# Kernel tuning notes

Measured on AMD Instinct MI355X. Metric: run time of the kernel, lower is better.

Reference implementation:

```python
import jax, jax.numpy as jnp
import numpy as np

N_NODES = 524288
N_EDGES = 786432
NUM_GRAPHS = 8192
NUM_NODE_TYPES = 16
NODE_DIM = 256
EDGE_DIM = 128
OUT_DIM = 1


def setup_inputs() -> dict:
    key = jax.random.key(0)
    ks = jax.random.split(key, 12)
    h_node = jax.random.uniform(ks[0], (N_NODES, NUM_NODE_TYPES), dtype=jnp.float32)
    pos_node = jax.random.normal(ks[1], (N_NODES, 3), dtype=jnp.float32)
    batch_node = jnp.sort(jax.random.randint(ks[2], (N_NODES,), 0, NUM_GRAPHS)).astype(jnp.int64)
    edge_index = jax.random.randint(ks[3], (2, N_EDGES), 0, N_NODES).astype(jnp.int64)
    batch_edge = jnp.sort(jax.random.randint(ks[4], (N_EDGES,), 0, NUM_GRAPHS)).astype(jnp.int64)
    s = 0.05
    W_node = jax.random.normal(ks[5], (NUM_NODE_TYPES, NODE_DIM), dtype=jnp.float32) * s
    W_edge = jax.random.normal(ks[6], (2 * NUM_NODE_TYPES, EDGE_DIM), dtype=jnp.float32) * s
    H = NODE_DIM + EDGE_DIM
    W1 = jax.random.normal(ks[7], (H, H), dtype=jnp.float32) * s
    b1 = jnp.zeros((H,), dtype=jnp.float32)
    W2 = jax.random.normal(ks[8], (H, OUT_DIM), dtype=jnp.float32) * s
    b2 = jnp.zeros((OUT_DIM,), dtype=jnp.float32)
    return {"h_node": h_node, "pos_node": pos_node, "batch_node": batch_node,
            "edge_index": edge_index, "batch_edge": batch_edge,
            "W_node": W_node, "W_edge": W_edge, "W1": W1, "b1": b1, "W2": W2, "b2": b2}


def _segment_mean(x, seg_ids, num_segments):
    # fused replacement for the original per-graph boolean-mask loop:
    # h[seg==k].mean(0) for all k, via one scatter-add + count normalize
    sums = jax.ops.segment_sum(x, seg_ids, num_segments=num_segments)
    cnts = jax.ops.segment_sum(jnp.ones((x.shape[0],), x.dtype), seg_ids, num_segments=num_segments)
    return sums / jnp.maximum(cnts, 1.0)[:, None]


def reference(h_node, pos_node, batch_node, edge_index, batch_edge,
              W_node, W_edge, W1, b1, W2, b2):
    # h_edge = cat(h_node[src], h_node[dst])  -> [E, 2*num_node_types]
    h_edge_raw = jnp.concatenate([h_node[edge_index[0]], h_node[edge_index[1]]], axis=-1)
    # num_timesteps == 0 path: plain embedders, no time embedding
    hn = h_node @ W_node          # [N, node_dim]
    he = h_edge_raw @ W_edge      # [E, edge_dim]
    # encoder treated as identity (NodeEdgeNet not in scope); pooling is the target op
    node_mean = _segment_mean(hn, batch_node, NUM_GRAPHS)  # [G, node_dim]
    edge_mean = _segment_mean(he, batch_edge, NUM_GRAPHS)  # [G, edge_dim]
    h_sub = jnp.concatenate([node_mean, edge_mean], axis=-1)  # [G, node_dim+edge_dim]
    # final MLP (num_layer=2): Linear -> ReLU -> Linear
    pred = jax.nn.relu(h_sub @ W1 + b1) @ W2 + b2  # [G, 1]
    return pred
```

## Files before the change

### kernel.cpp

```cpp
#include <hip/hip_runtime.h>

#define N_NODES_C   524288
#define N_EDGES_C   786432
#define NUM_GRAPHS_C 8192
#define NT 16
#define NODE_DIM_C 256
#define EDGE_DIM_C 128
#define HDIM 384
#define KC 48

#define KR_GRAPH_BLOCKS 2048
#define KR_FOLD_BLOCKS  72
#define KR_BLOCKS (KR_GRAPH_BLOCKS + KR_FOLD_BLOCKS)
#define NODE_BLOCKS 2048
#define EDGE_BLOCKS 16384
#define EDGE_BASE   NODE_BLOCKS
#define KM_BLOCKS   (NODE_BLOCKS + EDGE_BLOCKS)

#define WS_NM    0
#define WS_EM8   524288
#define WS_WC    8912896
#define WS_NS    8986624
#define WS_DESC  9019456
#define WS_ECNT  10068032
#define WS_REC   10100800

__device__ __forceinline__ void f4_add(float4& a, const float4 v) {
    a.x += v.x; a.y += v.y; a.z += v.z; a.w += v.w;
}

__device__ __forceinline__ void f4_shfl_xor_add(float4& a, int mask) {
    a.x += __shfl_xor(a.x, mask, 64);
    a.y += __shfl_xor(a.y, mask, 64);
    a.z += __shfl_xor(a.z, mask, 64);
    a.w += __shfl_xor(a.w, mask, 64);
}

__device__ __forceinline__ int lower_bound_i32(const int* __restrict__ a, int n, int key) {
    int lo = 0, hi = n;
    while (lo < hi) {
        int mid = (lo + hi) >> 1;
        if (a[mid] < key) lo = mid + 1; else hi = mid;
    }
    return lo;
}

__device__ __forceinline__ void wave_seg_bounds(const int* __restrict__ b, int n,
                                                int g, int lane, int& s, int& e) {
    int key = g + ((lane >= 32) ? 1 : 0);
    int lo = lower_bound_i32(b, n, key);
    s = __shfl(lo, 0, 64);
    e = __shfl(lo, 32, 64);
}

__global__ __launch_bounds__(256) void kr_build(
    const int* __restrict__ bnode, const int* __restrict__ bedge,
    const int* __restrict__ esrc, const int* __restrict__ edst,
    const float* __restrict__ Wn, const float* __restrict__ We,
    const float* __restrict__ W1,
    int* __restrict__ rec, int4* __restrict__ desc,
    int* __restrict__ ecnt, int* __restrict__ nstart, float* __restrict__ Wc) {
    int tid = threadIdx.x, blk = blockIdx.x;

    if (blk >= KR_GRAPH_BLOCKS) {
        int o = (blk - KR_GRAPH_BLOCKS) * 256 + tid;
        if (o >= KC * HDIM) return;
        int k = o / HDIM, j = o % HDIM;
        float acc = 0.f;
        if (k < NT) {
            const float* wr = &Wn[k * NODE_DIM_C];
            #pragma unroll 16
            for (int kk = 0; kk < NODE_DIM_C; ++kk)
                acc = fmaf(wr[kk], W1[(size_t)kk * HDIM + j], acc);
        } else {
            const float* wr = &We[(k - NT) * EDGE_DIM_C];
            #pragma unroll 16
            for (int kk = 0; kk < EDGE_DIM_C; ++kk)
                acc = fmaf(wr[kk], W1[(size_t)(NODE_DIM_C + kk) * HDIM + j], acc);
        }
        Wc[o] = acc;
        return;
    }

    int i = blk * 256 + tid;
    {
        int g0 = bnode[i];
        int hi = (i + 1 < N_NODES_C) ? bnode[i + 1] : NUM_GRAPHS_C;
        if (i == 0) for (int g = 0; g <= g0; ++g) nstart[g] = 0;
        for (int g = g0 + 1; g <= hi; ++g) nstart[g] = i + 1;
    }

    int wave = tid >> 6, lane = tid & 63;
    int g = blk * 4 + wave;
    int s, e;
    wave_seg_bounds(bedge, N_EDGES_C, g, lane, s, e);
    int cnt = e - s;
    if (lane == 0) ecnt[g] = cnt;

    __shared__ int lcnt[4][16];
    __shared__ int lcur[4][16];
    if (lane < 16) lcnt[wave][lane] = 0;
    for (int q = s + lane; q < e; q += 64) {
        int a = esrc[q];
        atomicAdd(&lcnt[wave][((a >> 16) << 1) + 0], 1);
        int b = edst[q];
        atomicAdd(&lcnt[wave][((b >> 16) << 1) + 1], 1);
    }
    int c = (lane < 16) ? lcnt[wave][lane] : 0;
    int incl = c;
    #pragma unroll
    for (int d = 1; d < 16; d <<= 1) {
        int v = __shfl_up(incl, d, 64);
        if (lane >= d) incl += v;
    }
    int excl = incl - c;
    if (lane < 16) lcur[wave][lane] = excl;
    int i0 = (lane < 8) ? 2 * lane : 0;
    int i1 = (lane < 8) ? 2 * lane + 1 : 0;
    int i2 = (lane < 7) ? 2 * lane + 2 : 0;
    int b0 = __shfl(excl, i0, 64);
    int b1 = __shfl(excl, i1, 64);
    int e1 = __shfl(excl, i2, 64);
    if (lane < 8) {
        int e1a = (lane == 7) ? 2 * s + 2 * cnt : 2 * s + e1;
        desc[(g << 3) + lane] = make_int4(2 * s + b0, 2 * s + b1, e1a, cnt);
    }
    for (int q = s + lane; q < e; q += 64) {
        int a = esrc[q];
        int pa = atomicAdd(&lcur[wave][((a >> 16) << 1) + 0], 1);
        rec[2 * s + pa] = a;
        int b = edst[q];
        int pb = atomicAdd(&lcur[wave][((b >> 16) << 1) + 1], 1);
        rec[2 * s + pb] = b;
    }
}

__global__ __launch_bounds__(256) void km_mega(
    const float* __restrict__ h_node,
    const int* __restrict__ nstart, const int4* __restrict__ desc,
    const int* __restrict__ rec,
    float* __restrict__ nm, float* __restrict__ em8) {
    int blk  = blockIdx.x;
    int wave = threadIdx.x >> 6;
    int lane = threadIdx.x & 63;
    const float4* h4 = (const float4*)h_node;
    const float4 z4 = make_float4(0.f, 0.f, 0.f, 0.f);

    if (blk < EDGE_BASE) {
        int s8 = blk & 7;
        int g  = s8 * 1024 + (blk >> 3) * 4 + wave;
        int s = nstart[g], e = nstart[g + 1];
        int row_off = lane >> 2;
        int quad    = lane & 3;
        float4 a0 = z4, a1 = z4;
        int i = s + row_off;
        for (; i + 16 < e; i += 32) {
            float4 v0 = h4[(size_t)i * 4 + quad];
            float4 v1 = h4[(size_t)(i + 16) * 4 + quad];
            f4_add(a0, v0);
            f4_add(a1, v1);
        }
        if (i < e) f4_add(a0, h4[(size_t)i * 4 + quad]);
        f4_add(a0, a1);
        f4_shfl_xor_add(a0, 4);
        f4_shfl_xor_add(a0, 8);
        f4_shfl_xor_add(a0, 16);
        f4_shfl_xor_add(a0, 32);
        if (row_off == 0) {
            float inv = 1.f / fmaxf((float)(e - s), 1.f);
            ((float4*)nm)[(size_t)g * 4 + quad] =
                make_float4(a0.x * inv, a0.y * inv, a0.z * inv, a0.w * inv);
        }
    } else {
        int r     = blk - EDGE_BASE;
        int slice = r & 7;
        int g     = (r >> 3) * 4 + wave;
        int4 d    = desc[(g << 3) + slice];
        int slot = lane >> 3;
        int p    = (lane >> 2) & 1;
        int quad = lane & 3;
        int st = p ? d.y : d.x;
        int en = p ? d.z : d.y;
        int cmax = max(d.y - d.x, d.z - d.y);
        int T = (cmax + 7) >> 3;
        float4 acc = z4;
        int i = st + slot;
        int idx = (i < en) ? rec[i] : -1;
        for (int t = 1; t < T; ++t) {
            int i2 = i + 8;
            int nx = (i2 < en) ? rec[i2] : -1;
            if (idx >= 0) f4_add(acc, h4[(size_t)idx * 4 + quad]);
            idx = nx; i = i2;
        }
        if (idx >= 0) f4_add(acc, h4[(size_t)idx * 4 + quad]);
        f4_shfl_xor_add(acc, 8);
        f4_shfl_xor_add(acc, 16);
        f4_shfl_xor_add(acc, 32);
        if (slot == 0) {
            ((float4*)em8)[((size_t)(g * 8 + slice)) * 8 + p * 4 + quad] = acc;
        }
    }
}

#define GPB 16
__global__ __launch_bounds__(HDIM) void k3_mlp(
    const float* __restrict__ nm, const float* __restrict__ em8,
    const int* __restrict__ ecnt,
    const float* __restrict__ Wc, const float* __restrict__ b1,
    const float* __restrict__ W2, const float* __restrict__ b2,
    float* __restrict__ pred) {
    int j = threadIdx.x;
    float wc[KC];
    #pragma unroll
    for (int k = 0; k < KC; ++k) wc[k] = Wc[k * HDIM + j];
    float b1j = b1[j], w2j = W2[j], b20 = b2[0];

    __shared__ float fs[GPB][KC];
    __shared__ float part[GPB][6];
    int g0 = blockIdx.x * GPB;
    for (int t = j; t < GPB * KC; t += HDIM) {
        int g = t / KC, k = t % KC;
        int G = g0 + g;
        float val;
        if (k < NT) {
            val = nm[(size_t)G * NT + k];
        } else {
            float ssum = 0.f;
            #pragma unroll
            for (int s = 0; s < 8; ++s)
                ssum += em8[((size_t)(G * 8 + s)) * 32 + (k - NT)];
            val = ssum / fmaxf((float)ecnt[G], 1.f);
        }
        fs[g][k] = val;
    }
    __syncthreads();

    int wave = j >> 6, lane = j & 63;
    for (int g = 0; g < GPB; ++g) {
        float z = b1j;
        #pragma unroll
        for (int k = 0; k < KC; ++k) z = fmaf(fs[g][k], wc[k], z);
        z = fmaxf(z, 0.f);
        float p = z * w2j;
        #pragma unroll
        for (int off = 32; off > 0; off >>= 1) p += __shfl_down(p, off, 64);
        if (lane == 0) part[g][wave] = p;
    }
    __syncthreads();
    if (j < GPB) {
        float sacc = b20;
        #pragma unroll
        for (int w = 0; w < 6; ++w) sacc += part[j][w];
        pred[g0 + j] = sacc;
    }
}

extern "C" void kernel_launch(void* const* d_in, const int* in_sizes, int n_in,
                              void* d_out, int out_size, void* d_ws, size_t ws_size,
                              hipStream_t stream) {
    const float* h_node     = (const float*)d_in[0];
    const int*   batch_node = (const int*)d_in[2];
    const int*   edge_index = (const int*)d_in[3];
    const int*   batch_edge = (const int*)d_in[4];
    const float* W_node     = (const float*)d_in[5];
    const float* W_edge     = (const float*)d_in[6];
    const float* W1         = (const float*)d_in[7];
    const float* b1         = (const float*)d_in[8];
    const float* W2         = (const float*)d_in[9];
    const float* b2         = (const float*)d_in[10];
    float* pred = (float*)d_out;

    char* ws = (char*)d_ws;
    float* nm     = (float*)(ws + WS_NM);
    float* em8    = (float*)(ws + WS_EM8);
    float* Wc     = (float*)(ws + WS_WC);
    int*   nstart = (int*)(ws + WS_NS);
    int4*  desc   = (int4*)(ws + WS_DESC);
    int*   ecnt   = (int*)(ws + WS_ECNT);
    int*   rec    = (int*)(ws + WS_REC);

    const int* esrc = edge_index;
    const int* edst = edge_index + N_EDGES_C;

    kr_build<<<KR_BLOCKS, 256, 0, stream>>>(
        batch_node, batch_edge, esrc, edst, W_node, W_edge, W1,
        rec, desc, ecnt, nstart, Wc);
    km_mega <<<KM_BLOCKS, 256, 0, stream>>>(
        h_node, nstart, desc, rec, nm, em8);
    k3_mlp  <<<NUM_GRAPHS_C / GPB, HDIM, 0, stream>>>(
        nm, em8, ecnt, Wc, b1, W2, b2, pred);
}
```

Baseline: 150.0 us.

## Fuse node segment-mean into build kernel using binary-searched node bounds

```diff
diff --git a/kernel.cpp b/kernel.cpp
--- a/kernel.cpp
+++ b/kernel.cpp
@@ -9,21 +9,17 @@
 #define HDIM 384
 #define KC 48
 
-#define KR_GRAPH_BLOCKS 2048
-#define KR_FOLD_BLOCKS  72
-#define KR_BLOCKS (KR_GRAPH_BLOCKS + KR_FOLD_BLOCKS)
-#define NODE_BLOCKS 2048
-#define EDGE_BLOCKS 16384
-#define EDGE_BASE   NODE_BLOCKS
-#define KM_BLOCKS   (NODE_BLOCKS + EDGE_BLOCKS)
+#define KP_GRAPH_BLOCKS 2048
+#define KP_FOLD_BLOCKS  72
+#define KP_BLOCKS (KP_GRAPH_BLOCKS + KP_FOLD_BLOCKS)
+#define KE_BLOCKS 16384
 
 #define WS_NM    0
 #define WS_EM8   524288
 #define WS_WC    8912896
-#define WS_NS    8986624
-#define WS_DESC  9019456
-#define WS_ECNT  10068032
-#define WS_REC   10100800
+#define WS_DESC  8986624
+#define WS_ECNT  10035200
+#define WS_REC   10067968
 
 __device__ __forceinline__ void f4_add(float4& a, const float4 v) {
     a.x += v.x; a.y += v.y; a.z += v.z; a.w += v.w;
@@ -45,25 +41,18 @@
     return lo;
 }
 
-__device__ __forceinline__ void wave_seg_bounds(const int* __restrict__ b, int n,
-                                                int g, int lane, int& s, int& e) {
-    int key = g + ((lane >= 32) ? 1 : 0);
-    int lo = lower_bound_i32(b, n, key);
-    s = __shfl(lo, 0, 64);
-    e = __shfl(lo, 32, 64);
-}
-
-__global__ __launch_bounds__(256) void kr_build(
+__global__ __launch_bounds__(256) void kp_build(
     const int* __restrict__ bnode, const int* __restrict__ bedge,
     const int* __restrict__ esrc, const int* __restrict__ edst,
+    const float* __restrict__ h_node,
     const float* __restrict__ Wn, const float* __restrict__ We,
     const float* __restrict__ W1,
-    int* __restrict__ rec, int4* __restrict__ desc,
-    int* __restrict__ ecnt, int* __restrict__ nstart, float* __restrict__ Wc) {
+    int* __restrict__ rec, int4* __restrict__ desc, int* __restrict__ ecnt,
+    float* __restrict__ nm, float* __restrict__ Wc) {
     int tid = threadIdx.x, blk = blockIdx.x;
 
-    if (blk >= KR_GRAPH_BLOCKS) {
-        int o = (blk - KR_GRAPH_BLOCKS) * 256 + tid;
+    if (blk >= KP_GRAPH_BLOCKS) {
+        int o = (blk - KP_GRAPH_BLOCKS) * 256 + tid;
         if (o >= KC * HDIM) return;
         int k = o / HDIM, j = o % HDIM;
         float acc = 0.f;
@@ -82,25 +71,64 @@
         return;
     }
 
-    int i = blk * 256 + tid;
+    int wave = tid >> 6, lane = tid & 63;
+    int s8 = blk & 7;
+    int g  = s8 * 1024 + (blk >> 3) * 4 + wave;
+    const float4* h4 = (const float4*)h_node;
+    const float4 z4 = make_float4(0.f, 0.f, 0.f, 0.f);
+
     {
-        int g0 = bnode[i];
-        int hi = (i + 1 < N_NODES_C) ? bnode[i + 1] : NUM_GRAPHS_C;
-        if (i == 0) for (int g = 0; g <= g0; ++g) nstart[g] = 0;
-        for (int g = g0 + 1; g <= hi; ++g) nstart[g] = i + 1;
-    }
-
-    int wave = tid >> 6, lane = tid & 63;
-    int g = blk * 4 + wave;
-    int s, e;
-    wave_seg_bounds(bedge, N_EDGES_C, g, lane, s, e);
-    int cnt = e - s;
+        const int* arr = (lane & 32) ? bnode : bedge;
+        int n   = (lane & 32) ? N_NODES_C : N_EDGES_C;
+        int key = g + ((lane >> 4) & 1);
+        int lo = lower_bound_i32(arr, n, key);
+        __shared__ int bb[4][4];
+        if ((lane & 15) == 0) bb[wave][lane >> 4] = lo;
+    }
+    __builtin_amdgcn_s_waitcnt(0);
+    __shared__ int bbx[4][4];
+    int es, ee, ns, ne;
+    {
+        const int* arr = (lane & 32) ? bnode : bedge;
+        int n   = (lane & 32) ? N_NODES_C : N_EDGES_C;
+        int key = g + ((lane >> 4) & 1);
+        int lo = lower_bound_i32(arr, n, key);
+        es = __shfl(lo, 0, 64);
+        ee = __shfl(lo, 16, 64);
+        ns = __shfl(lo, 32, 64);
+        ne = __shfl(lo, 48, 64);
+    }
+    int cnt = ee - es;
     if (lane == 0) ecnt[g] = cnt;
+
+    {
+        int row_off = lane >> 2;
+        int quad    = lane & 3;
+        float4 a0 = z4, a1 = z4;
+        int i = ns + row_off;
+        for (; i + 16 < ne; i += 32) {
+            float4 v0 = h4[(size_t)i * 4 + quad];
+            float4 v1 = h4[(size_t)(i + 16) * 4 + quad];
+            f4_add(a0, v0);
+            f4_add(a1, v1);
+        }
+        if (i < ne) f4_add(a0, h4[(size_t)i * 4 + quad]);
+        f4_add(a0, a1);
+        f4_shfl_xor_add(a0, 4);
+        f4_shfl_xor_add(a0, 8);
+        f4_shfl_xor_add(a0, 16);
+        f4_shfl_xor_add(a0, 32);
+        if (row_off == 0) {
+            float inv = 1.f / fmaxf((float)(ne - ns), 1.f);
+            ((float4*)nm)[(size_t)g * 4 + quad] =
+                make_float4(a0.x * inv, a0.y * inv, a0.z * inv, a0.w * inv);
+        }
+    }
 
     __shared__ int lcnt[4][16];
     __shared__ int lcur[4][16];
     if (lane < 16) lcnt[wave][lane] = 0;
-    for (int q = s + lane; q < e; q += 64) {
+    for (int q = es + lane; q < ee; q += 64) {
         int a = esrc[q];
         atomicAdd(&lcnt[wave][((a >> 16) << 1) + 0], 1);
         int b = edst[q];
@@ -122,83 +150,54 @@
     int b1 = __shfl(excl, i1, 64);
     int e1 = __shfl(excl, i2, 64);
     if (lane < 8) {
-        int e1a = (lane == 7) ? 2 * s + 2 * cnt : 2 * s + e1;
-        desc[(g << 3) + lane] = make_int4(2 * s + b0, 2 * s + b1, e1a, cnt);
-    }
-    for (int q = s + lane; q < e; q += 64) {
+        int e1a = (lane == 7) ? 2 * es + 2 * cnt : 2 * es + e1;
+        desc[(g << 3) + lane] = make_int4(2 * es + b0, 2 * es + b1, e1a, cnt);
+    }
+    for (int q = es + lane; q < ee; q += 64) {
         int a = esrc[q];
         int pa = atomicAdd(&lcur[wave][((a >> 16) << 1) + 0], 1);
-        rec[2 * s + pa] = a;
+        rec[2 * es + pa] = a;
         int b = edst[q];
         int pb = atomicAdd(&lcur[wave][((b >> 16) << 1) + 1], 1);
-        rec[2 * s + pb] = b;
-    }
-}
-
-__global__ __launch_bounds__(256) void km_mega(
+        rec[2 * es + pb] = b;
+    }
+}
+
+__global__ __launch_bounds__(256) void ke_edge(
     const float* __restrict__ h_node,
-    const int* __restrict__ nstart, const int4* __restrict__ desc,
-    const int* __restrict__ rec,
-    float* __restrict__ nm, float* __restrict__ em8) {
+    const int4* __restrict__ desc, const int* __restrict__ rec,
+    float* __restrict__ em8) {
     int blk  = blockIdx.x;
     int wave = threadIdx.x >> 6;
     int lane = threadIdx.x & 63;
     const float4* h4 = (const float4*)h_node;
     const float4 z4 = make_float4(0.f, 0.f, 0.f, 0.f);
 
-    if (blk < EDGE_BASE) {
-        int s8 = blk & 7;
-        int g  = s8 * 1024 + (blk >> 3) * 4 + wave;
-        int s = nstart[g], e = nstart[g + 1];
-        int row_off = lane >> 2;
-        int quad    = lane & 3;
-        float4 a0 = z4, a1 = z4;
-        int i = s + row_off;
-        for (; i + 16 < e; i += 32) {
-            float4 v0 = h4[(size_t)i * 4 + quad];
-            float4 v1 = h4[(size_t)(i + 16) * 4 + quad];
-            f4_add(a0, v0);
-            f4_add(a1, v1);
-        }
-        if (i < e) f4_add(a0, h4[(size_t)i * 4 + quad]);
-        f4_add(a0, a1);
-        f4_shfl_xor_add(a0, 4);
-        f4_shfl_xor_add(a0, 8);
-        f4_shfl_xor_add(a0, 16);
-        f4_shfl_xor_add(a0, 32);
-        if (row_off == 0) {
-            float inv = 1.f / fmaxf((float)(e - s), 1.f);
-            ((float4*)nm)[(size_t)g * 4 + quad] =
-                make_float4(a0.x * inv, a0.y * inv, a0.z * inv, a0.w * inv);
-        }
-    } else {
-        int r     = blk - EDGE_BASE;
-        int slice = r & 7;
-        int g     = (r >> 3) * 4 + wave;
-        int4 d    = desc[(g << 3) + slice];
-        int slot = lane >> 3;
-        int p    = (lane >> 2) & 1;
-        int quad = lane & 3;
-        int st = p ? d.y : d.x;
-        int en = p ? d.z : d.y;
-        int cmax = max(d.y - d.x, d.z - d.y);
-        int T = (cmax + 7) >> 3;
-        float4 acc = z4;
-        int i = st + slot;
-        int idx = (i < en) ? rec[i] : -1;
-        for (int t = 1; t < T; ++t) {
-            int i2 = i + 8;
-            int nx = (i2 < en) ? rec[i2] : -1;
-            if (idx >= 0) f4_add(acc, h4[(size_t)idx * 4 + quad]);
-            idx = nx; i = i2;
-        }
+    int slice = blk & 7;
+    int g     = (blk >> 3) * 4 + wave;
+    int4 d    = desc[(g << 3) + slice];
+    int slot = lane >> 3;
+    int p    = (lane >> 2) & 1;
+    int quad = lane & 3;
+    int st = p ? d.y : d.x;
+    int en = p ? d.z : d.y;
+    int cmax = max(d.y - d.x, d.z - d.y);
+    int T = (cmax + 7) >> 3;
+    float4 acc = z4;
+    int i = st + slot;
+    int idx = (i < en) ? rec[i] : -1;
+    for (int t = 1; t < T; ++t) {
+        int i2 = i + 8;
+        int nx = (i2 < en) ? rec[i2] : -1;
         if (idx >= 0) f4_add(acc, h4[(size_t)idx * 4 + quad]);
-        f4_shfl_xor_add(acc, 8);
-        f4_shfl_xor_add(acc, 16);
-        f4_shfl_xor_add(acc, 32);
-        if (slot == 0) {
-            ((float4*)em8)[((size_t)(g * 8 + slice)) * 8 + p * 4 + quad] = acc;
-        }
+        idx = nx; i = i2;
+    }
+    if (idx >= 0) f4_add(acc, h4[(size_t)idx * 4 + quad]);
+    f4_shfl_xor_add(acc, 8);
+    f4_shfl_xor_add(acc, 16);
+    f4_shfl_xor_add(acc, 32);
+    if (slot == 0) {
+        ((float4*)em8)[((size_t)(g * 8 + slice)) * 8 + p * 4 + quad] = acc;
     }
 }
 
@@ -271,22 +270,20 @@
     float* pred = (float*)d_out;
 
     char* ws = (char*)d_ws;
-    float* nm     = (float*)(ws + WS_NM);
-    float* em8    = (float*)(ws + WS_EM8);
-    float* Wc     = (float*)(ws + WS_WC);
-    int*   nstart = (int*)(ws + WS_NS);
-    int4*  desc   = (int4*)(ws + WS_DESC);
-    int*   ecnt   = (int*)(ws + WS_ECNT);
-    int*   rec    = (int*)(ws + WS_REC);
+    float* nm   = (float*)(ws + WS_NM);
+    float* em8  = (float*)(ws + WS_EM8);
+    float* Wc   = (float*)(ws + WS_WC);
+    int4*  desc = (int4*)(ws + WS_DESC);
+    int*   ecnt = (int*)(ws + WS_ECNT);
+    int*   rec  = (int*)(ws + WS_REC);
 
     const int* esrc = edge_index;
     const int* edst = edge_index + N_EDGES_C;
 
-    kr_build<<<KR_BLOCKS, 256, 0, stream>>>(
-        batch_node, batch_edge, esrc, edst, W_node, W_edge, W1,
-        rec, desc, ecnt, nstart, Wc);
-    km_mega <<<KM_BLOCKS, 256, 0, stream>>>(
-        h_node, nstart, desc, rec, nm, em8);
+    kp_build<<<KP_BLOCKS, 256, 0, stream>>>(
+        batch_node, batch_edge, esrc, edst, h_node, W_node, W_edge, W1,
+        rec, desc, ecnt, nm, Wc);
+    ke_edge <<<KE_BLOCKS, 256, 0, stream>>>(h_node, desc, rec, em8);
     k3_mlp  <<<NUM_GRAPHS_C / GPB, HDIM, 0, stream>>>(
         nm, em8, ecnt, Wc, b1, W2, b2, pred);
 }
```

After: 149.3 us. Within noise of the previous version (-0.5%).

## Move weight-folding blocks into gather kernel and make em8 slice-major

Applied to the files above, without the earlier changes.

```diff
diff --git a/kernel.cpp b/kernel.cpp
--- a/kernel.cpp
+++ b/kernel.cpp
@@ -9,21 +9,20 @@
 #define HDIM 384
 #define KC 48
 
-#define KR_GRAPH_BLOCKS 2048
-#define KR_FOLD_BLOCKS  72
-#define KR_BLOCKS (KR_GRAPH_BLOCKS + KR_FOLD_BLOCKS)
+#define FOLD_BLOCKS 72
 #define NODE_BLOCKS 2048
 #define EDGE_BLOCKS 16384
-#define EDGE_BASE   NODE_BLOCKS
-#define KM_BLOCKS   (NODE_BLOCKS + EDGE_BLOCKS)
+#define NODE_BASE   FOLD_BLOCKS
+#define EDGE_BASE   (FOLD_BLOCKS + NODE_BLOCKS)
+#define TOTAL_BLOCKS (FOLD_BLOCKS + NODE_BLOCKS + EDGE_BLOCKS)
 
 #define WS_NM    0
 #define WS_EM8   524288
 #define WS_WC    8912896
 #define WS_NS    8986624
-#define WS_DESC  9019456
-#define WS_ECNT  10068032
-#define WS_REC   10100800
+#define WS_ECNT  9019456
+#define WS_DESC  9052288
+#define WS_REC   10100864
 
 __device__ __forceinline__ void f4_add(float4& a, const float4 v) {
     a.x += v.x; a.y += v.y; a.z += v.z; a.w += v.w;
@@ -56,14 +55,77 @@
 __global__ __launch_bounds__(256) void kr_build(
     const int* __restrict__ bnode, const int* __restrict__ bedge,
     const int* __restrict__ esrc, const int* __restrict__ edst,
+    int* __restrict__ rec, int4* __restrict__ desc,
+    int* __restrict__ ecnt, int* __restrict__ nstart) {
+    int tid = threadIdx.x, blk = blockIdx.x;
+    int i = blk * 256 + tid;
+    {
+        int g0 = bnode[i];
+        int hi = (i + 1 < N_NODES_C) ? bnode[i + 1] : NUM_GRAPHS_C;
+        if (i == 0) for (int g = 0; g <= g0; ++g) nstart[g] = 0;
+        for (int g = g0 + 1; g <= hi; ++g) nstart[g] = i + 1;
+    }
+
+    int wave = tid >> 6, lane = tid & 63;
+    int g = blk * 4 + wave;
+    int s, e;
+    wave_seg_bounds(bedge, N_EDGES_C, g, lane, s, e);
+    int cnt = e - s;
+    if (lane == 0) ecnt[g] = cnt;
+
+    __shared__ int lcnt[4][16];
+    __shared__ int lcur[4][16];
+    if (lane < 16) lcnt[wave][lane] = 0;
+    for (int q = s + lane; q < e; q += 64) {
+        int a = esrc[q];
+        atomicAdd(&lcnt[wave][((a >> 16) << 1) + 0], 1);
+        int b = edst[q];
+        atomicAdd(&lcnt[wave][((b >> 16) << 1) + 1], 1);
+    }
+    int c = (lane < 16) ? lcnt[wave][lane] : 0;
+    int incl = c;
+    #pragma unroll
+    for (int d = 1; d < 16; d <<= 1) {
+        int v = __shfl_up(incl, d, 64);
+        if (lane >= d) incl += v;
+    }
+    int excl = incl - c;
+    if (lane < 16) lcur[wave][lane] = excl;
+    int i0 = (lane < 8) ? 2 * lane : 0;
+    int i1 = (lane < 8) ? 2 * lane + 1 : 0;
+    int i2 = (lane < 7) ? 2 * lane + 2 : 0;
+    int b0 = __shfl(excl, i0, 64);
+    int b1 = __shfl(excl, i1, 64);
+    int e1 = __shfl(excl, i2, 64);
+    if (lane < 8) {
+        int e1a = (lane == 7) ? 2 * s + 2 * cnt : 2 * s + e1;
+        desc[(g << 3) + lane] = make_int4(2 * s + b0, 2 * s + b1, e1a, cnt);
+    }
+    for (int q = s + lane; q < e; q += 64) {
+        int a = esrc[q];
+        int pa = atomicAdd(&lcur[wave][((a >> 16) << 1) + 0], 1);
+        rec[2 * s + pa] = a;
+        int b = edst[q];
+        int pb = atomicAdd(&lcur[wave][((b >> 16) << 1) + 1], 1);
+        rec[2 * s + pb] = b;
+    }
+}
+
+__global__ __launch_bounds__(256) void km_mega(
+    const float* __restrict__ h_node,
+    const int* __restrict__ nstart, const int4* __restrict__ desc,
+    const int* __restrict__ rec,
     const float* __restrict__ Wn, const float* __restrict__ We,
     const float* __restrict__ W1,
-    int* __restrict__ rec, int4* __restrict__ desc,
-    int* __restrict__ ecnt, int* __restrict__ nstart, float* __restrict__ Wc) {
-    int tid = threadIdx.x, blk = blockIdx.x;
-
-    if (blk >= KR_GRAPH_BLOCKS) {
-        int o = (blk - KR_GRAPH_BLOCKS) * 256 + tid;
+    float* __restrict__ nm, float* __restrict__ em8, float* __restrict__ Wc) {
+    int blk  = blockIdx.x;
+    int wave = threadIdx.x >> 6;
+    int lane = threadIdx.x & 63;
+    const float4* h4 = (const float4*)h_node;
+    const float4 z4 = make_float4(0.f, 0.f, 0.f, 0.f);
+
+    if (blk < FOLD_BLOCKS) {
+        int o = blk * 256 + threadIdx.x;
         if (o >= KC * HDIM) return;
         int k = o / HDIM, j = o % HDIM;
         float acc = 0.f;
@@ -79,76 +141,10 @@
                 acc = fmaf(wr[kk], W1[(size_t)(NODE_DIM_C + kk) * HDIM + j], acc);
         }
         Wc[o] = acc;
-        return;
-    }
-
-    int i = blk * 256 + tid;
-    {
-        int g0 = bnode[i];
-        int hi = (i + 1 < N_NODES_C) ? bnode[i + 1] : NUM_GRAPHS_C;
-        if (i == 0) for (int g = 0; g <= g0; ++g) nstart[g] = 0;
-        for (int g = g0 + 1; g <= hi; ++g) nstart[g] = i + 1;
-    }
-
-    int wave = tid >> 6, lane = tid & 63;
-    int g = blk * 4 + wave;
-    int s, e;
-    wave_seg_bounds(bedge, N_EDGES_C, g, lane, s, e);
-    int cnt = e - s;
-    if (lane == 0) ecnt[g] = cnt;
-
-    __shared__ int lcnt[4][16];
-    __shared__ int lcur[4][16];
-    if (lane < 16) lcnt[wave][lane] = 0;
-    for (int q = s + lane; q < e; q += 64) {
-        int a = esrc[q];
-        atomicAdd(&lcnt[wave][((a >> 16) << 1) + 0], 1);
-        int b = edst[q];
-        atomicAdd(&lcnt[wave][((b >> 16) << 1) + 1], 1);
-    }
-    int c = (lane < 16) ? lcnt[wave][lane] : 0;
-    int incl = c;
-    #pragma unroll
-    for (int d = 1; d < 16; d <<= 1) {
-        int v = __shfl_up(incl, d, 64);
-        if (lane >= d) incl += v;
-    }
-    int excl = incl - c;
-    if (lane < 16) lcur[wave][lane] = excl;
-    int i0 = (lane < 8) ? 2 * lane : 0;
-    int i1 = (lane < 8) ? 2 * lane + 1 : 0;
-    int i2 = (lane < 7) ? 2 * lane + 2 : 0;
-    int b0 = __shfl(excl, i0, 64);
-    int b1 = __shfl(excl, i1, 64);
-    int e1 = __shfl(excl, i2, 64);
-    if (lane < 8) {
-        int e1a = (lane == 7) ? 2 * s + 2 * cnt : 2 * s + e1;
-        desc[(g << 3) + lane] = make_int4(2 * s + b0, 2 * s + b1, e1a, cnt);
-    }
-    for (int q = s + lane; q < e; q += 64) {
-        int a = esrc[q];
-        int pa = atomicAdd(&lcur[wave][((a >> 16) << 1) + 0], 1);
-        rec[2 * s + pa] = a;
-        int b = edst[q];
-        int pb = atomicAdd(&lcur[wave][((b >> 16) << 1) + 1], 1);
-        rec[2 * s + pb] = b;
-    }
-}
-
-__global__ __launch_bounds__(256) void km_mega(
-    const float* __restrict__ h_node,
-    const int* __restrict__ nstart, const int4* __restrict__ desc,
-    const int* __restrict__ rec,
-    float* __restrict__ nm, float* __restrict__ em8) {
-    int blk  = blockIdx.x;
-    int wave = threadIdx.x >> 6;
-    int lane = threadIdx.x & 63;
-    const float4* h4 = (const float4*)h_node;
-    const float4 z4 = make_float4(0.f, 0.f, 0.f, 0.f);
-
-    if (blk < EDGE_BASE) {
-        int s8 = blk & 7;
-        int g  = s8 * 1024 + (blk >> 3) * 4 + wave;
+    } else if (blk < EDGE_BASE) {
+        int r = blk - NODE_BASE;
+        int s8 = r & 7;
+        int g  = s8 * 1024 + (r >> 3) * 4 + wave;
         int s = nstart[g], e = nstart[g + 1];
         int row_off = lane >> 2;
         int quad    = lane & 3;
@@ -197,7 +193,7 @@
         f4_shfl_xor_add(acc, 16);
         f4_shfl_xor_add(acc, 32);
         if (slot == 0) {
-            ((float4*)em8)[((size_t)(g * 8 + slice)) * 8 + p * 4 + quad] = acc;
+            ((float4*)em8)[((size_t)(slice * NUM_GRAPHS_C + g)) * 8 + p * 4 + quad] = acc;
         }
     }
 }
@@ -228,7 +224,7 @@
             float ssum = 0.f;
             #pragma unroll
             for (int s = 0; s < 8; ++s)
-                ssum += em8[((size_t)(G * 8 + s)) * 32 + (k - NT)];
+                ssum += em8[((size_t)(s * NUM_GRAPHS_C + G)) * 32 + (k - NT)];
             val = ssum / fmaxf((float)ecnt[G], 1.f);
         }
         fs[g][k] = val;
@@ -275,18 +271,17 @@
     float* em8    = (float*)(ws + WS_EM8);
     float* Wc     = (float*)(ws + WS_WC);
     int*   nstart = (int*)(ws + WS_NS);
+    int*   ecnt   = (int*)(ws + WS_ECNT);
     int4*  desc   = (int4*)(ws + WS_DESC);
-    int*   ecnt   = (int*)(ws + WS_ECNT);
     int*   rec    = (int*)(ws + WS_REC);
 
     const int* esrc = edge_index;
     const int* edst = edge_index + N_EDGES_C;
 
-    kr_build<<<KR_BLOCKS, 256, 0, stream>>>(
-        batch_node, batch_edge, esrc, edst, W_node, W_edge, W1,
-        rec, desc, ecnt, nstart, Wc);
-    km_mega <<<KM_BLOCKS, 256, 0, stream>>>(
-        h_node, nstart, desc, rec, nm, em8);
+    kr_build<<<NUM_GRAPHS_C / 4, 256, 0, stream>>>(
+        batch_node, batch_edge, esrc, edst, rec, desc, ecnt, nstart);
+    km_mega <<<TOTAL_BLOCKS, 256, 0, stream>>>(
+        h_node, nstart, desc, rec, W_node, W_edge, W1, nm, em8, Wc);
     k3_mlp  <<<NUM_GRAPHS_C / GPB, HDIM, 0, stream>>>(
         nm, em8, ecnt, Wc, b1, W2, b2, pred);
 }
```

Result: faster. 145.1 us (-3.3%).
